# Performance work log

Hardware: AMD Instinct MI355X
Metric: run time of the kernel (lower is better)

The kernel has to match this reference:

```python
import jax, jax.numpy as jnp
import numpy as np

B, S, E = 8, 1024, 1024
H, HS = 16, 64  # num_heads, head_size; H*HS == E


def setup_inputs() -> dict:
    key = jax.random.key(0)
    ks = jax.random.split(key, 6)
    scale = 1.0 / np.sqrt(E)
    x = jax.random.normal(ks[0], (B, S, E), dtype=jnp.float32)
    # per-head projection weights stacked: [H, E, HS] (Linear(n_embd, head_size, bias=False))
    Wq = jax.random.normal(ks[1], (H, E, HS), dtype=jnp.float32) * scale
    Wk = jax.random.normal(ks[2], (H, E, HS), dtype=jnp.float32) * scale
    Wv = jax.random.normal(ks[3], (H, E, HS), dtype=jnp.float32) * scale
    # output projection Linear(n_embd, n_embd): torch weight [out, in] plus bias
    Wproj = jax.random.normal(ks[4], (E, E), dtype=jnp.float32) * scale
    bproj = jax.random.normal(ks[5], (E,), dtype=jnp.float32) * scale
    return {"x": x, "Wq": Wq, "Wk": Wk, "Wv": Wv, "Wproj": Wproj, "bproj": bproj}


def reference(x, Wq, Wk, Wv, Wproj, bproj):
    # q,k,v: [B, H, S, HS]
    q = jnp.einsum('bse,hed->bhsd', x, Wq)
    k = jnp.einsum('bse,hed->bhsd', x, Wk)
    v = jnp.einsum('bse,hed->bhsd', x, Wv)
    scores = jnp.einsum('bhsd,bhtd->bhst', q, k) * (HS ** -0.5)  # [B,H,S,S]
    causal = jnp.tril(jnp.ones((S, S), dtype=bool))
    scores = jnp.where(causal, scores, jnp.finfo(scores.dtype).min)
    attn = jax.nn.softmax(scores, axis=-1)
    out = jnp.einsum('bhst,bhtd->bhsd', attn, v)         # [B,H,S,HS]
    out = out.transpose(0, 2, 1, 3).reshape(B, S, H * HS)  # concat heads -> [B,S,E]
    return out @ Wproj.T + bproj  # dropout p=0 is identity
```

## Files before the change

kernel.cpp:

```cpp
#include <hip/hip_runtime.h>
#include <stdint.h>

#define DEVI __device__ __forceinline__

typedef __attribute__((ext_vector_type(8))) short bf16x8;
typedef __attribute__((ext_vector_type(4))) float floatx4;
typedef __attribute__((ext_vector_type(16))) float floatx16;

constexpr int Bb = 8, Ss = 1024, Ee = 1024, Hh = 16, HSs = 64;
constexpr int Mq = Bb * Ss;
constexpr int Nqkv = 3 * Hh * HSs;
constexpr int Kd = Ee;

DEVI unsigned short f2bf(float x) {
  union { float f; uint32_t u; } v; v.f = x;
  uint32_t r = v.u + 0x7FFFu + ((v.u >> 16) & 1u);
  return (unsigned short)(r >> 16);
}

DEVI uint32_t cvtpk(float a, float b) {
  uint32_t r;
  asm("v_cvt_pk_bf16_f32 %0, %1, %2" : "=v"(r) : "v"(a), "v"(b));
  return r;
}

DEVI bf16x8 mkfrag(uint32_t a, uint32_t b, uint32_t c, uint32_t d) {
  union { uint32_t u[4]; bf16x8 v; } x;
  x.u[0] = a; x.u[1] = b; x.u[2] = c; x.u[3] = d;
  return x.v;
}

DEVI floatx4 mfma16(bf16x8 a, bf16x8 b, floatx4 c) {
  return __builtin_amdgcn_mfma_f32_16x16x32_bf16(a, b, c, 0, 0, 0);
}
DEVI floatx16 mfma32(bf16x8 a, bf16x8 b, floatx16 c) {
  return __builtin_amdgcn_mfma_f32_32x32x16_bf16(a, b, c, 0, 0, 0);
}

DEVI void gload_lds16(const void* g, void* l) {
  __builtin_amdgcn_global_load_lds(
      (const __attribute__((address_space(1))) uint32_t*)(uintptr_t)g,
      (__attribute__((address_space(3))) uint32_t*)(uint32_t)(uintptr_t)l,
      16, 0, 0);
}

__global__ void cvt_fused(const float* __restrict__ x, const float* __restrict__ Wproj,
                          const float* __restrict__ Wq, const float* __restrict__ Wk,
                          const float* __restrict__ Wv,
                          unsigned short* __restrict__ xb, unsigned short* __restrict__ wprojb,
                          unsigned short* __restrict__ wqkvb) {
  __shared__ float tile[64][65];
  const int bid = blockIdx.x;
  if (bid < 9216) {
    const float* in; unsigned short* out; int i;
    if (bid < 8192) { in = x;     out = xb;     i = (bid * 256 + threadIdx.x) * 4; }
    else            { in = Wproj; out = wprojb; i = ((bid - 8192) * 256 + threadIdx.x) * 4; }
    float4 v = *(const float4*)&in[i];
    ushort4 o;
    o.x = f2bf(v.x); o.y = f2bf(v.y); o.z = f2bf(v.z); o.w = f2bf(v.w);
    *(ushort4*)(void*)&out[i] = o;
    return;
  }
  const int idx = bid - 9216;
  const int k0 = (idx & 15) * 64;
  const int hh = idx >> 4;
  const int qkv = hh >> 4, h = hh & 15;
  const float* W = (qkv == 0) ? Wq : ((qkv == 1) ? Wk : Wv);
  const float scale = (qkv == 0) ? (0.125f * 1.44269504f) : 1.0f;
  const float* src = W + (size_t)h * Ee * HSs;
  const int c = threadIdx.x & 63, r4 = threadIdx.x >> 6;
#pragma unroll
  for (int rr = 0; rr < 16; ++rr) {
    int row = rr * 4 + r4;
    tile[row][c] = src[(size_t)(k0 + row) * HSs + c] * scale;
  }
  __syncthreads();
  const int base_n = qkv * 1024 + h * 64;
#pragma unroll
  for (int rr = 0; rr < 16; ++rr) {
    int hs = rr * 4 + r4;
    wqkvb[(size_t)(base_n + hs) * Kd + k0 + c] = f2bf(tile[c][hs]);
  }
}

__global__ __launch_bounds__(256, 2) void gemm_qkv(
    const unsigned short* __restrict__ A, const unsigned short* __restrict__ Bt,
    unsigned short* __restrict__ Qb, unsigned short* __restrict__ Kb,
    unsigned short* __restrict__ Vtb, int Kdim) {
  __shared__ __align__(16) unsigned short As[128 * 64];
  __shared__ __align__(16) unsigned short Bs[128 * 64];
  const int tid = threadIdx.x;
  const int lane = tid & 63;
  const int wid = tid >> 6;
  const int wm = wid >> 1, wn = wid & 1;
  const int m0 = blockIdx.y * 128;
  const int n0 = blockIdx.x * 128;

  floatx4 acc[4][4];
#pragma unroll
  for (int i = 0; i < 4; ++i)
#pragma unroll
    for (int j = 0; j < 4; ++j) acc[i][j] = (floatx4)0.f;

  const int srow = lane >> 3;
  const int schunk = (lane & 7) ^ srow;

  for (int kt = 0; kt < Kdim; kt += 64) {
#pragma unroll
    for (int j = 0; j < 4; ++j) {
      const int g = wid * 4 + j;
      const int row = g * 8 + srow;
      gload_lds16(A + (size_t)(m0 + row) * Kdim + kt + schunk * 8, &As[g * 8 * 64]);
      gload_lds16(Bt + (size_t)(n0 + row) * Kdim + kt + schunk * 8, &Bs[g * 8 * 64]);
    }
    __syncthreads();
#pragma unroll
    for (int kk = 0; kk < 2; ++kk) {
      const int c = kk * 4 + (lane >> 4);
      bf16x8 af[4], bf[4];
#pragma unroll
      for (int i = 0; i < 4; ++i) {
        const int ra = wm * 64 + i * 16 + (lane & 15);
        af[i] = *(const bf16x8*)&As[ra * 64 + ((c ^ (ra & 7)) << 3)];
        const int rb = wn * 64 + i * 16 + (lane & 15);
        bf[i] = *(const bf16x8*)&Bs[rb * 64 + ((c ^ (rb & 7)) << 3)];
      }
#pragma unroll
      for (int i = 0; i < 4; ++i)
#pragma unroll
        for (int j = 0; j < 4; ++j) acc[i][j] = mfma16(af[i], bf[j], acc[i][j]);
    }
    __syncthreads();
  }

  const int mrow0 = m0 + wm * 64 + ((lane >> 4) << 2);
  const int ncol0 = n0 + wn * 64 + (lane & 15);
#pragma unroll
  for (int i = 0; i < 4; ++i) {
#pragma unroll
    for (int j = 0; j < 4; ++j) {
      const int n = ncol0 + j * 16;
      const int qkv = n >> 10;
      const int h = (n & 1023) >> 6;
      const int hs = n & 63;
#pragma unroll
      for (int r = 0; r < 4; ++r) {
        const int m = mrow0 + i * 16 + r;
        const int b = m >> 10, s = m & 1023;
        const unsigned short bv = f2bf(acc[i][j][r]);
        if (qkv == 0)
          Qb[(((size_t)b * Hh + h) * Ss + s) * HSs + hs] = bv;
        else if (qkv == 1)
          Kb[(((size_t)b * Hh + h) * Ss + s) * HSs + hs] = bv;
        else
          Vtb[(((size_t)b * Hh + h) * HSs + hs) * Ss + s] = bv;
      }
    }
  }
}

__global__ __launch_bounds__(256, 2) void gemm_proj(
    const unsigned short* __restrict__ A, const unsigned short* __restrict__ Bt,
    float* __restrict__ Out, const float* __restrict__ bias, int Ndim, int Kdim) {
  __shared__ __align__(16) unsigned short As[128 * 64];
  __shared__ __align__(16) unsigned short Bs[128 * 64];
  const int tid = threadIdx.x;
  const int lane = tid & 63;
  const int wid = tid >> 6;
  const int wm = wid >> 1, wn = wid & 1;
  const int m0 = blockIdx.y * 128;
  const int n0 = blockIdx.x * 128;

  floatx4 acc[4][4];
#pragma unroll
  for (int i = 0; i < 4; ++i)
#pragma unroll
    for (int j = 0; j < 4; ++j) acc[i][j] = (floatx4)0.f;

  const int srow = lane >> 3;
  const int schunk = (lane & 7) ^ srow;

  for (int kt = 0; kt < Kdim; kt += 64) {
#pragma unroll
    for (int j = 0; j < 4; ++j) {
      const int g = wid * 4 + j;
      const int row = g * 8 + srow;
      gload_lds16(A + (size_t)(m0 + row) * Kdim + kt + schunk * 8, &As[g * 8 * 64]);
      gload_lds16(Bt + (size_t)(n0 + row) * Kdim + kt + schunk * 8, &Bs[g * 8 * 64]);
    }
    __syncthreads();
#pragma unroll
    for (int kk = 0; kk < 2; ++kk) {
      const int c = kk * 4 + (lane >> 4);
      bf16x8 af[4], bf[4];
#pragma unroll
      for (int i = 0; i < 4; ++i) {
        const int ra = wm * 64 + i * 16 + (lane & 15);
        af[i] = *(const bf16x8*)&As[ra * 64 + ((c ^ (ra & 7)) << 3)];
        const int rb = wn * 64 + i * 16 + (lane & 15);
        bf[i] = *(const bf16x8*)&Bs[rb * 64 + ((c ^ (rb & 7)) << 3)];
      }
#pragma unroll
      for (int i = 0; i < 4; ++i)
#pragma unroll
        for (int j = 0; j < 4; ++j) acc[i][j] = mfma16(af[i], bf[j], acc[i][j]);
    }
    __syncthreads();
  }

  const int mrow0 = m0 + wm * 64 + ((lane >> 4) << 2);
  const int ncol0 = n0 + wn * 64 + (lane & 15);
#pragma unroll
  for (int j = 0; j < 4; ++j) {
    const int n = ncol0 + j * 16;
    const float bj = bias[n];
#pragma unroll
    for (int i = 0; i < 4; ++i) {
#pragma unroll
      for (int r = 0; r < 4; ++r) {
        const int m = mrow0 + i * 16 + r;
        Out[(size_t)m * Ndim + n] = acc[i][j][r] + bj;
      }
    }
  }
}

__global__ __launch_bounds__(512, 4) void attn(
    const unsigned short* __restrict__ Qb, const unsigned short* __restrict__ Kb,
    const unsigned short* __restrict__ Vtb, unsigned short* __restrict__ Ob) {
  __shared__ __align__(16) unsigned short Ks[3][64 * 64];
  __shared__ __align__(16) unsigned short Vs[3][64 * 64];

  const int tid = threadIdx.x;
  const int lane = tid & 63;
  const int wid = tid >> 6;
  const int ln = lane & 31;
  const int hi = lane >> 5;
  const int bh = blockIdx.x & 127;
  const int qs = blockIdx.x >> 7;
  const int q0 = (3 - qs) * 256;
  const int bI = bh >> 4, hI = bh & 15;
  const unsigned short* Qp = Qb + (size_t)bh * Ss * HSs;
  const unsigned short* Kp = Kb + (size_t)bh * Ss * HSs;
  const unsigned short* Vp = Vtb + (size_t)bh * HSs * Ss;
  const int qw = q0 + wid * 32;
  const int q = qw + ln;

  bf16x8 qf[4];
#pragma unroll
  for (int kc = 0; kc < 4; ++kc)
    qf[kc] = *(const bf16x8*)&Qp[(size_t)q * 64 + kc * 16 + hi * 8];

  floatx16 oacc[2];
  oacc[0] = (floatx16)0.f;
  oacc[1] = (floatx16)0.f;
  float mrow = -3.0e38f, lrow = 0.f;

  const int srow = lane >> 3;
  const int schunk = (lane & 7) ^ srow;
  const int nt = (q0 >> 6) + 4;

  auto stageKV = [&](int t, int b) {
    const int row = wid * 8 + srow;
    gload_lds16(Kp + (size_t)(t * 64 + row) * 64 + schunk * 8, &Ks[b][wid * 512]);
    gload_lds16(Vp + (size_t)row * Ss + t * 64 + schunk * 8, &Vs[b][wid * 512]);
  };

  stageKV(0, 0);
  stageKV(1, 1);
  asm volatile("s_waitcnt vmcnt(2)" ::: "memory");
  __builtin_amdgcn_s_barrier();

  for (int t = 0; t < nt; ++t) {
    const int cur = t % 3;
    const bool pf = (t + 2 < nt);
    if (pf) stageKV(t + 2, (t + 2) % 3);
    const int t0 = t * 64;

    if (t0 <= qw + 31) {
      const unsigned short* Kc = Ks[cur];
      const unsigned short* Vc = Vs[cur];
      floatx16 sc[2];
#pragma unroll
      for (int tt = 0; tt < 2; ++tt) {
        floatx16 s = (floatx16)0.f;
        __builtin_amdgcn_s_setprio(1);
#pragma unroll
        for (int kc = 0; kc < 4; ++kc) {
          const int row = tt * 32 + ln;
          bf16x8 kf = *(const bf16x8*)&Kc[row * 64 + ((((kc << 1) | hi) ^ (ln & 7)) << 3)];
          s = mfma32(kf, qf[kc], s);
        }
        __builtin_amdgcn_s_setprio(0);
        sc[tt] = s;
      }
      if (t0 + 63 > qw) {
#pragma unroll
        for (int tt = 0; tt < 2; ++tt)
#pragma unroll
          for (int r = 0; r < 16; ++r) {
            const int tg = t0 + tt * 32 + (r & 3) + 8 * (r >> 2) + 4 * hi;
            if (tg > q) sc[tt][r] = -1e30f;
          }
      }
      float mx = sc[0][0];
#pragma unroll
      for (int tt = 0; tt < 2; ++tt)
#pragma unroll
        for (int r = 0; r < 16; ++r) mx = fmaxf(mx, sc[tt][r]);
      mx = fmaxf(mx, __shfl_xor(mx, 32));
      if (!__all(mx - mrow <= 8.0f)) {
        const float mnew = fmaxf(mrow, mx);
        const float scal = __builtin_amdgcn_exp2f(mrow - mnew);
        mrow = mnew;
        lrow *= scal;
#pragma unroll
        for (int dt = 0; dt < 2; ++dt)
#pragma unroll
          for (int r = 0; r < 16; ++r) oacc[dt][r] *= scal;
      }
      float ss = 0.f;
#pragma unroll
      for (int tt = 0; tt < 2; ++tt)
#pragma unroll
        for (int r = 0; r < 16; ++r) {
          const float p = __builtin_amdgcn_exp2f(sc[tt][r] - mrow);
          sc[tt][r] = p;
          ss += p;
        }
      ss += __shfl_xor(ss, 32);
      lrow += ss;

      bf16x8 pf_[4];
#pragma unroll
      for (int tt = 0; tt < 2; ++tt)
#pragma unroll
        for (int fb = 0; fb < 2; ++fb) {
          const int b = fb * 8;
          const uint32_t w0 = cvtpk(sc[tt][b + 0], sc[tt][b + 1]);
          const uint32_t w1 = cvtpk(sc[tt][b + 2], sc[tt][b + 3]);
          const uint32_t w2 = cvtpk(sc[tt][b + 4], sc[tt][b + 5]);
          const uint32_t w3 = cvtpk(sc[tt][b + 6], sc[tt][b + 7]);
          const uint32_t s0 = hi ? w0 : w2;
          const uint32_t s1 = hi ? w1 : w3;
          const uint32_t r0 = (uint32_t)__shfl_xor((int)s0, 32);
          const uint32_t r1 = (uint32_t)__shfl_xor((int)s1, 32);
          pf_[tt * 2 + fb] = mkfrag(hi ? r0 : w0, hi ? r1 : w1, hi ? w2 : r0, hi ? w3 : r1);
        }
#pragma unroll
      for (int dt = 0; dt < 2; ++dt) {
        const int row = dt * 32 + ln;
        __builtin_amdgcn_s_setprio(1);
#pragma unroll
        for (int kc = 0; kc < 4; ++kc) {
          bf16x8 vf = *(const bf16x8*)&Vc[row * 64 + ((((kc << 1) | hi) ^ (ln & 7)) << 3)];
          oacc[dt] = mfma32(vf, pf_[kc], oacc[dt]);
        }
        __builtin_amdgcn_s_setprio(0);
      }
    }

    if (pf) { asm volatile("s_waitcnt vmcnt(2)" ::: "memory"); }
    else    { asm volatile("s_waitcnt vmcnt(0)" ::: "memory"); }
    __builtin_amdgcn_s_barrier();
  }

  const float inv = 1.0f / lrow;
  unsigned short* Op = Ob + ((size_t)bI * Ss + q) * Ee + hI * 64;
#pragma unroll
  for (int dt = 0; dt < 2; ++dt)
#pragma unroll
    for (int g4 = 0; g4 < 4; ++g4) {
      ushort4 o;
      o.x = f2bf(oacc[dt][g4 * 4 + 0] * inv);
      o.y = f2bf(oacc[dt][g4 * 4 + 1] * inv);
      o.z = f2bf(oacc[dt][g4 * 4 + 2] * inv);
      o.w = f2bf(oacc[dt][g4 * 4 + 3] * inv);
      *(ushort4*)(void*)&Op[dt * 32 + g4 * 8 + hi * 4] = o;
    }
}

extern "C" void kernel_launch(void* const* d_in, const int* in_sizes, int n_in,
                              void* d_out, int out_size, void* d_ws, size_t ws_size,
                              hipStream_t stream) {
  const float* x = (const float*)d_in[0];
  const float* Wq = (const float*)d_in[1];
  const float* Wk = (const float*)d_in[2];
  const float* Wv = (const float*)d_in[3];
  const float* Wproj = (const float*)d_in[4];
  const float* bproj = (const float*)d_in[5];
  float* out = (float*)d_out;

  char* ws = (char*)d_ws;
  unsigned short* xb     = (unsigned short*)(ws);
  unsigned short* wqkvb  = (unsigned short*)(ws + (16u << 20));
  unsigned short* wprojb = (unsigned short*)(ws + (22u << 20));
  unsigned short* Qb     = (unsigned short*)(ws + (24u << 20));
  unsigned short* Kb     = (unsigned short*)(ws + (40u << 20));
  unsigned short* Vtb    = (unsigned short*)(ws + (56u << 20));
  unsigned short* Obuf   = (unsigned short*)(ws + (72u << 20));

  cvt_fused<<<9984, 256, 0, stream>>>(x, Wproj, Wq, Wk, Wv, xb, wprojb, wqkvb);
  gemm_qkv<<<dim3(Nqkv / 128, Mq / 128), 256, 0, stream>>>(
      xb, wqkvb, Qb, Kb, Vtb, Kd);
  attn<<<512, 512, 0, stream>>>(Qb, Kb, Vtb, Obuf);
  gemm_proj<<<dim3(Ee / 128, Mq / 128), 256, 0, stream>>>(
      Obuf, wprojb, out, bproj, Ee, Kd);
}
```

Baseline: 151.3 us.

## Enlarge QKV GEMM tile to 256x256 with double-buffered LDS prefetch

The QKV projection GEMM moves from 128x128 tiles with 4 waves to 256x256 tiles with 8 waves, each wave computing 128x64. LDS is double-buffered so the next K-slice is loaded by direct global-to-LDS loads while the current one is multiplied, with vmcnt waits and raw barriers instead of two syncthreads per step. MFMA sections are wrapped in s_setprio raises. This cuts global traffic per FLOP and hides load latency, but LDS rises to 128 KB and occupancy drops to one block per CU, with fewer blocks (384) to spread across CUs.

```diff
diff --git a/kernel.cpp b/kernel.cpp
--- a/kernel.cpp
+++ b/kernel.cpp
@@ -83,60 +83,79 @@
   }
 }
 
-__global__ __launch_bounds__(256, 2) void gemm_qkv(
+__global__ __launch_bounds__(512, 1) void gemm_qkv(
     const unsigned short* __restrict__ A, const unsigned short* __restrict__ Bt,
     unsigned short* __restrict__ Qb, unsigned short* __restrict__ Kb,
     unsigned short* __restrict__ Vtb, int Kdim) {
-  __shared__ __align__(16) unsigned short As[128 * 64];
-  __shared__ __align__(16) unsigned short Bs[128 * 64];
+  __shared__ __align__(16) unsigned short As[2][256 * 64];
+  __shared__ __align__(16) unsigned short Bs[2][256 * 64];
   const int tid = threadIdx.x;
   const int lane = tid & 63;
   const int wid = tid >> 6;
-  const int wm = wid >> 1, wn = wid & 1;
-  const int m0 = blockIdx.y * 128;
-  const int n0 = blockIdx.x * 128;
-
-  floatx4 acc[4][4];
-#pragma unroll
-  for (int i = 0; i < 4; ++i)
-#pragma unroll
-    for (int j = 0; j < 4; ++j) acc[i][j] = (floatx4)0.f;
-
+  const int wm = wid >> 2, wn = wid & 3;
+  const int m0 = blockIdx.y * 256;
+  const int n0 = blockIdx.x * 256;
   const int srow = lane >> 3;
   const int schunk = (lane & 7) ^ srow;
-
-  for (int kt = 0; kt < Kdim; kt += 64) {
+  const int NT = Kdim >> 6;
+
+  floatx4 acc[8][4];
+#pragma unroll
+  for (int i = 0; i < 8; ++i)
+#pragma unroll
+    for (int j = 0; j < 4; ++j) acc[i][j] = (floatx4)0.f;
+
+  auto stage = [&](int kt, int b) {
 #pragma unroll
     for (int j = 0; j < 4; ++j) {
-      const int g = wid * 4 + j;
+      const int g = wid + j * 8;
       const int row = g * 8 + srow;
-      gload_lds16(A + (size_t)(m0 + row) * Kdim + kt + schunk * 8, &As[g * 8 * 64]);
-      gload_lds16(Bt + (size_t)(n0 + row) * Kdim + kt + schunk * 8, &Bs[g * 8 * 64]);
-    }
-    __syncthreads();
+      gload_lds16(A + (size_t)(m0 + row) * Kdim + kt * 64 + schunk * 8, &As[b][g * 512]);
+      gload_lds16(Bt + (size_t)(n0 + row) * Kdim + kt * 64 + schunk * 8, &Bs[b][g * 512]);
+    }
+  };
+
+  stage(0, 0);
+
+  for (int kt = 0; kt < NT; ++kt) {
+    const int cur = kt & 1;
+    if (kt + 1 < NT) {
+      stage(kt + 1, cur ^ 1);
+      asm volatile("s_waitcnt vmcnt(8)" ::: "memory");
+    } else {
+      asm volatile("s_waitcnt vmcnt(0)" ::: "memory");
+    }
+    __builtin_amdgcn_s_barrier();
+    const unsigned short* Ap = As[cur];
+    const unsigned short* Bp = Bs[cur];
 #pragma unroll
     for (int kk = 0; kk < 2; ++kk) {
       const int c = kk * 4 + (lane >> 4);
-      bf16x8 af[4], bf[4];
-#pragma unroll
-      for (int i = 0; i < 4; ++i) {
-        const int ra = wm * 64 + i * 16 + (lane & 15);
-        af[i] = *(const bf16x8*)&As[ra * 64 + ((c ^ (ra & 7)) << 3)];
-        const int rb = wn * 64 + i * 16 + (lane & 15);
-        bf[i] = *(const bf16x8*)&Bs[rb * 64 + ((c ^ (rb & 7)) << 3)];
-      }
-#pragma unroll
-      for (int i = 0; i < 4; ++i)
+      bf16x8 af[8], bf[4];
+#pragma unroll
+      for (int i = 0; i < 8; ++i) {
+        const int ra = wm * 128 + i * 16 + (lane & 15);
+        af[i] = *(const bf16x8*)&Ap[ra * 64 + ((c ^ (ra & 7)) << 3)];
+      }
+#pragma unroll
+      for (int j = 0; j < 4; ++j) {
+        const int rb = wn * 64 + j * 16 + (lane & 15);
+        bf[j] = *(const bf16x8*)&Bp[rb * 64 + ((c ^ (rb & 7)) << 3)];
+      }
+      __builtin_amdgcn_s_setprio(1);
+#pragma unroll
+      for (int i = 0; i < 8; ++i)
 #pragma unroll
         for (int j = 0; j < 4; ++j) acc[i][j] = mfma16(af[i], bf[j], acc[i][j]);
-    }
-    __syncthreads();
-  }
-
-  const int mrow0 = m0 + wm * 64 + ((lane >> 4) << 2);
+      __builtin_amdgcn_s_setprio(0);
+    }
+    __builtin_amdgcn_s_barrier();
+  }
+
+  const int mrow0 = m0 + wm * 128 + ((lane >> 4) << 2);
   const int ncol0 = n0 + wn * 64 + (lane & 15);
 #pragma unroll
-  for (int i = 0; i < 4; ++i) {
+  for (int i = 0; i < 8; ++i) {
 #pragma unroll
     for (int j = 0; j < 4; ++j) {
       const int n = ncol0 + j * 16;
@@ -401,7 +420,7 @@
   unsigned short* Obuf   = (unsigned short*)(ws + (72u << 20));
 
   cvt_fused<<<9984, 256, 0, stream>>>(x, Wproj, Wq, Wk, Wv, xb, wprojb, wqkvb);
-  gemm_qkv<<<dim3(Nqkv / 128, Mq / 128), 256, 0, stream>>>(
+  gemm_qkv<<<dim3(Nqkv / 256, Mq / 256), 512, 0, stream>>>(
       xb, wqkvb, Qb, Kb, Vtb, Kd);
   attn<<<512, 512, 0, stream>>>(Qb, Kb, Vtb, Obuf);
   gemm_proj<<<dim3(Ee / 128, Mq / 128), 256, 0, stream>>>(
```

New measurement: 169.9 us. 12.3% more time.

## Widen QKV GEMM tile to 128x256 with 8 waves and vectorize V^T stores

Applied to the files above, without the earlier changes.

The QKV projection GEMM now uses 512-thread blocks covering a 128x256 output tile, with 8 waves in a 2x4 layout, so each block loads its A tile once for twice as many output columns. The epilogue hoists the Q/K/V selection to a per-block branch. For the transposed V output it writes four consecutive sequence positions as one ushort4 store instead of scattered 2-byte stores. The larger tile raises LDS use to 48KB per block and cuts the grid size, which may lower occupancy or leave CUs with uneven work.

```diff
diff --git a/kernel.cpp b/kernel.cpp
--- a/kernel.cpp
+++ b/kernel.cpp
@@ -83,35 +83,40 @@
   }
 }
 
-__global__ __launch_bounds__(256, 2) void gemm_qkv(
+__global__ __launch_bounds__(512, 3) void gemm_qkv(
     const unsigned short* __restrict__ A, const unsigned short* __restrict__ Bt,
     unsigned short* __restrict__ Qb, unsigned short* __restrict__ Kb,
     unsigned short* __restrict__ Vtb, int Kdim) {
   __shared__ __align__(16) unsigned short As[128 * 64];
-  __shared__ __align__(16) unsigned short Bs[128 * 64];
+  __shared__ __align__(16) unsigned short Bs[256 * 64];
   const int tid = threadIdx.x;
   const int lane = tid & 63;
   const int wid = tid >> 6;
-  const int wm = wid >> 1, wn = wid & 1;
+  const int wm = wid >> 2, wn = wid & 3;
   const int m0 = blockIdx.y * 128;
-  const int n0 = blockIdx.x * 128;
-
-  floatx4 acc[4][4];
-#pragma unroll
-  for (int i = 0; i < 4; ++i)
-#pragma unroll
-    for (int j = 0; j < 4; ++j) acc[i][j] = (floatx4)0.f;
-
+  const int n0 = blockIdx.x * 256;
   const int srow = lane >> 3;
   const int schunk = (lane & 7) ^ srow;
-
-  for (int kt = 0; kt < Kdim; kt += 64) {
-#pragma unroll
-    for (int j = 0; j < 4; ++j) {
-      const int g = wid * 4 + j;
+  const int NT = Kdim >> 6;
+
+  floatx4 acc[4][4];
+#pragma unroll
+  for (int i = 0; i < 4; ++i)
+#pragma unroll
+    for (int j = 0; j < 4; ++j) acc[i][j] = (floatx4)0.f;
+
+  for (int kt = 0; kt < NT; ++kt) {
+#pragma unroll
+    for (int i = 0; i < 2; ++i) {
+      const int g = wid + i * 8;
       const int row = g * 8 + srow;
-      gload_lds16(A + (size_t)(m0 + row) * Kdim + kt + schunk * 8, &As[g * 8 * 64]);
-      gload_lds16(Bt + (size_t)(n0 + row) * Kdim + kt + schunk * 8, &Bs[g * 8 * 64]);
+      gload_lds16(A + (size_t)(m0 + row) * Kdim + kt * 64 + schunk * 8, &As[g * 512]);
+    }
+#pragma unroll
+    for (int i = 0; i < 4; ++i) {
+      const int g = wid + i * 8;
+      const int row = g * 8 + srow;
+      gload_lds16(Bt + (size_t)(n0 + row) * Kdim + kt * 64 + schunk * 8, &Bs[g * 512]);
     }
     __syncthreads();
 #pragma unroll
@@ -135,25 +140,40 @@
 
   const int mrow0 = m0 + wm * 64 + ((lane >> 4) << 2);
   const int ncol0 = n0 + wn * 64 + (lane & 15);
-#pragma unroll
-  for (int i = 0; i < 4; ++i) {
-#pragma unroll
-    for (int j = 0; j < 4; ++j) {
-      const int n = ncol0 + j * 16;
-      const int qkv = n >> 10;
-      const int h = (n & 1023) >> 6;
-      const int hs = n & 63;
-#pragma unroll
-      for (int r = 0; r < 4; ++r) {
-        const int m = mrow0 + i * 16 + r;
-        const int b = m >> 10, s = m & 1023;
-        const unsigned short bv = f2bf(acc[i][j][r]);
-        if (qkv == 0)
-          Qb[(((size_t)b * Hh + h) * Ss + s) * HSs + hs] = bv;
-        else if (qkv == 1)
-          Kb[(((size_t)b * Hh + h) * Ss + s) * HSs + hs] = bv;
-        else
-          Vtb[(((size_t)b * Hh + h) * HSs + hs) * Ss + s] = bv;
+  const int qkv = n0 >> 10;
+  if (qkv == 2) {
+#pragma unroll
+    for (int i = 0; i < 4; ++i) {
+      const int m = mrow0 + i * 16;
+      const int b = m >> 10, s = m & 1023;
+#pragma unroll
+      for (int j = 0; j < 4; ++j) {
+        const int n = ncol0 + j * 16;
+        const int h = (n & 1023) >> 6;
+        const int hs = n & 63;
+        ushort4 o;
+        o.x = f2bf(acc[i][j][0]);
+        o.y = f2bf(acc[i][j][1]);
+        o.z = f2bf(acc[i][j][2]);
+        o.w = f2bf(acc[i][j][3]);
+        *(ushort4*)(void*)&Vtb[(((size_t)b * Hh + h) * HSs + hs) * Ss + s] = o;
+      }
+    }
+  } else {
+    unsigned short* P = (qkv == 0) ? Qb : Kb;
+#pragma unroll
+    for (int i = 0; i < 4; ++i) {
+#pragma unroll
+      for (int j = 0; j < 4; ++j) {
+        const int n = ncol0 + j * 16;
+        const int h = (n & 1023) >> 6;
+        const int hs = n & 63;
+#pragma unroll
+        for (int r = 0; r < 4; ++r) {
+          const int m = mrow0 + i * 16 + r;
+          const int b = m >> 10, s = m & 1023;
+          P[(((size_t)b * Hh + h) * Ss + s) * HSs + hs] = f2bf(acc[i][j][r]);
+        }
       }
     }
   }
@@ -401,7 +421,7 @@
   unsigned short* Obuf   = (unsigned short*)(ws + (72u << 20));
 
   cvt_fused<<<9984, 256, 0, stream>>>(x, Wproj, Wq, Wk, Wv, xb, wprojb, wqkvb);
-  gemm_qkv<<<dim3(Nqkv / 128, Mq / 128), 256, 0, stream>>>(
+  gemm_qkv<<<dim3(Nqkv / 256, Mq / 128), 512, 0, stream>>>(
       xb, wqkvb, Qb, Kb, Vtb, Kd);
   attn<<<512, 512, 0, stream>>>(Qb, Kb, Vtb, Obuf);
   gemm_proj<<<dim3(Ee / 128, Mq / 128), 256, 0, stream>>>(
```

New measurement: 153.5 us. No clear change (+1.4%).
